# Performance work log

Measured on AMD Instinct MI355X. Metric: run time of the kernel, lower is better.

The kernel has to match this reference:

```python
import jax, jax.numpy as jnp
import numpy as np

N = 50000
E = 1600000
F_IN = 256
DIMS = 64
N_CLS = 16
R = 8


def glorot(key, shape):
    fan = shape[-2] + shape[-1] if len(shape) >= 2 else shape[-1] * 2
    std = jnp.sqrt(6.0 / fan)
    return jax.random.uniform(key, shape, jnp.float32, -std, std)


def setup_inputs() -> dict:
    key = jax.random.key(0)
    ks = jax.random.split(key, 12)
    x = jax.random.normal(ks[0], (N, F_IN), jnp.float32)
    edge_index = jax.random.randint(ks[1], (2, E), 0, N)
    edge_weight = jax.random.uniform(ks[2], (E,), jnp.float32)
    edge_color = jax.random.randint(ks[3], (E,), 0, R)
    W1 = glorot(ks[4], (R, F_IN, DIMS))
    atten1 = glorot(ks[5], (R, 2 * DIMS))
    root1 = glorot(ks[6], (F_IN, DIMS))
    bias1 = jnp.zeros((DIMS,), jnp.float32)
    W2 = glorot(ks[7], (R, DIMS, N_CLS))
    atten2 = glorot(ks[8], (R, 2 * N_CLS))
    root2 = glorot(ks[9], (DIMS, N_CLS))
    bias2 = jnp.zeros((N_CLS,), jnp.float32)
    return dict(x=x, edge_index=edge_index, edge_weight=edge_weight,
                edge_color=edge_color, W1=W1, atten1=atten1, root1=root1,
                bias1=bias1, W2=W2, atten2=atten2, root2=root2, bias2=bias2)


def wrgat_conv(x, src, dst, ew, ec, W, atten, root, bias):
    # x: [N, f_in]; W: [R, f_in, d]; atten: [R, 2d]
    d = W.shape[-1]
    xr = jnp.einsum('nf,rfd->rnd', x, W)            # [R, N, d] per-relation projection
    xi = xr[ec, dst]                                 # [E, d] dst (x_i)
    xj = xr[ec, src]                                 # [E, d] src (x_j)
    a_i = atten[:, :d][ec]                           # [E, d]
    a_j = atten[:, d:][ec]
    s = jnp.sum(a_i * xi + a_j * xj, axis=-1)        # [E]
    s = jax.nn.leaky_relu(s, 0.2)
    # segment softmax over (relation, destination) groups
    seg = ec * N + dst                               # [E], each edge belongs to one relation
    nseg = R * N
    m = jax.ops.segment_max(s, seg, num_segments=nseg)
    m = jnp.where(jnp.isfinite(m), m, 0.0)           # empty segments -> 0
    e = jnp.exp(s - m[seg])
    denom = jax.ops.segment_sum(e, seg, num_segments=nseg)
    alpha = e / jnp.maximum(denom[seg], 1e-16)
    msg = (alpha * ew)[:, None] * xj                 # [E, d]
    summed = jax.ops.segment_sum(msg, seg, num_segments=nseg).reshape(R, N, d)
    cnt = jax.ops.segment_sum(jnp.ones_like(ew), seg, num_segments=nseg).reshape(R, N, 1)
    out = (summed / jnp.maximum(cnt, 1.0)).sum(axis=0)  # mean aggr per relation, summed over relations
    return out + x @ root + bias


def reference(x, edge_index, edge_weight, edge_color, W1, atten1, root1, bias1,
              W2, atten2, root2, bias2):
    src, dst = edge_index[0], edge_index[1]          # PyG flow source_to_target: x_j=src, x_i=dst
    h = wrgat_conv(x, src, dst, edge_weight, edge_color, W1, atten1, root1, bias1)
    h = jax.nn.relu(h)                               # dropout p=0 -> identity
    h = wrgat_conv(h, src, dst, edge_weight, edge_color, W2, atten2, root2, bias2)
    return jax.nn.log_softmax(h, axis=1)
```

## Files before the change

### kernel.cpp

```cpp
#include <hip/hip_runtime.h>
#include <math.h>

#define N_NODES 50000
#define N_EDGES 1600000
#define F_IN    256
#define DIMS    64
#define N_CLS   16
#define R_REL   8
#define CAP     96

#define PROJ_BLKS 3519
#define CSR_BLKS  3125
#define FRONT_BLKS (PROJ_BLKS + CSR_BLKS)

typedef short bf16x8 __attribute__((ext_vector_type(8)));
typedef float f32x4  __attribute__((ext_vector_type(4)));
typedef unsigned int u32;
typedef const __attribute__((address_space(1))) u32* gas_ptr;
typedef __attribute__((address_space(3))) u32* las_ptr;

__device__ __forceinline__ void async16(const void* g, void* l) {
    __builtin_amdgcn_global_load_lds((gas_ptr)g, (las_ptr)l, 16, 0, 0);
}

__device__ __forceinline__ unsigned short f2bf(float f) {
    unsigned u = __float_as_uint(f);
    unsigned r = (u + 0x7fffu + ((u >> 16) & 1u)) >> 16;
    return (unsigned short)r;
}
__device__ __forceinline__ float bf2f(unsigned short u) {
    return __uint_as_float(((unsigned)u) << 16);
}

__global__ __launch_bounds__(256) void cvt_x_kernel(
        const float* __restrict__ x, ushort* __restrict__ xb) {
    int i4 = blockIdx.x * 256 + threadIdx.x;
    float4 v = ((const float4*)x)[i4];
    ushort4 o;
    o.x = f2bf(v.x); o.y = f2bf(v.y); o.z = f2bf(v.z); o.w = f2bf(v.w);
    ((ushort4*)xb)[i4] = o;
}

__global__ __launch_bounds__(256) void cvt_w_kernel(
        const float* __restrict__ W1, const float* __restrict__ root1,
        ushort* __restrict__ wt1) {
    int idx = blockIdx.x * 256 + threadIdx.x;
    int r = idx >> 14, rem = idx & 16383;
    int n = rem >> 8, k = rem & 255;
    float v = (r < 8) ? W1[((size_t)r * F_IN + k) * DIMS + n]
                      : root1[(size_t)k * DIMS + n];
    wt1[idx] = f2bf(v);
}

#define BM 128
__global__ __launch_bounds__(256, 6) void front_kernel(
        const ushort* __restrict__ xb, const ushort* __restrict__ wt1,
        const float* __restrict__ at1,
        ushort* __restrict__ xr1b, float* __restrict__ hroot,
        float* __restrict__ si1, float* __restrict__ sj1,
        const int* __restrict__ ei, const int* __restrict__ ecol,
        const float* __restrict__ ew, int* __restrict__ fill,
        unsigned long long* __restrict__ rec) {
    __shared__ ushort xs[BM * 64];
    const int bid = blockIdx.x;
    const int t = threadIdx.x;

    int pb = -1, cb = -1;
    if (bid < 2 * CSR_BLKS) { if (bid & 1) cb = bid >> 1; else pb = bid >> 1; }
    else pb = CSR_BLKS + (bid - 2 * CSR_BLKS);

    if (cb >= 0) {
        int idx = cb * 256 + t;
        int2  s2 = ((const int2*)ei)[idx];
        int2  d2 = ((const int2*)(ei + N_EDGES))[idx];
        int2  c2 = ((const int2*)ecol)[idx];
        float2 w2 = ((const float2*)ew)[idx];
        int p0 = atomicAdd(&fill[d2.x], 1);
        int p1 = atomicAdd(&fill[d2.y], 1);
        unsigned long long r0 =
            ((unsigned long long)__float_as_uint(w2.x) << 32)
            | (unsigned)(s2.x | (c2.x << 16));
        unsigned long long r1 =
            ((unsigned long long)__float_as_uint(w2.y) << 32)
            | (unsigned)(s2.y | (c2.y << 16));
        int i0 = (p0 < CAP) ? d2.x * CAP + p0 : N_NODES * CAP;
        int i1 = (p1 < CAP) ? d2.y * CAP + p1 : N_NODES * CAP;
        __builtin_nontemporal_store(r0, &rec[i0]);
        __builtin_nontemporal_store(r1, &rec[i1]);
        return;
    }

    const int r = pb / 391;
    const int node0 = (pb % 391) * BM;
    const ushort* wrow = wt1 + (size_t)r * 64 * 256;

    const int w = t >> 6, lane = t & 63;
    const int lane15 = lane & 15, quad = lane >> 4;
    const int row0 = w * 32 + lane15;
    const int sw0 = row0 & 7;

    f32x4 acc[2][4];
    #pragma unroll
    for (int a = 0; a < 2; ++a)
        #pragma unroll
        for (int b = 0; b < 4; ++b)
            acc[a][b] = (f32x4){0.f, 0.f, 0.f, 0.f};

    for (int s = 0; s < 4; ++s) {
        __syncthreads();
        #pragma unroll
        for (int c = 0; c < 4; ++c) {
            int slot = c * 256 + t;
            int row = slot >> 3, k8p = slot & 7;
            int k8 = k8p ^ (row & 7);
            int node = node0 + row;
            if (node >= N_NODES) node = N_NODES - 1;
            async16(&xb[(size_t)node * 256 + s * 64 + k8 * 8],
                    &xs[(c * 256 + w * 64) * 8]);
        }
        __syncthreads();
        #pragma unroll
        for (int kk = 0; kk < 2; ++kk) {
            int k8 = kk * 4 + quad;
            int aidx = row0 * 64 + ((k8 ^ sw0) << 3);
            bf16x8 a0 = *(const bf16x8*)&xs[aidx];
            bf16x8 a1 = *(const bf16x8*)&xs[aidx + 16 * 64];
            int kg = s * 64 + kk * 32 + quad * 8;
            #pragma unroll
            for (int nt = 0; nt < 4; ++nt) {
                bf16x8 b = *(const bf16x8*)&wrow[(size_t)(nt * 16 + lane15) * 256 + kg];
                acc[0][nt] = __builtin_amdgcn_mfma_f32_16x16x32_bf16(a0, b, acc[0][nt], 0, 0, 0);
                acc[1][nt] = __builtin_amdgcn_mfma_f32_16x16x32_bf16(a1, b, acc[1][nt], 0, 0, 0);
            }
        }
    }

    const float* at = at1 + r * 128;
    #pragma unroll
    for (int mt = 0; mt < 2; ++mt) {
        float pi[4] = {0.f, 0.f, 0.f, 0.f};
        float pj[4] = {0.f, 0.f, 0.f, 0.f};
        #pragma unroll
        for (int nt = 0; nt < 4; ++nt) {
            int gcol = nt * 16 + lane15;
            float ai = 0.f, aj = 0.f;
            if (r < 8) { ai = at[gcol]; aj = at[64 + gcol]; }
            #pragma unroll
            for (int reg = 0; reg < 4; ++reg) {
                float v = acc[mt][nt][reg];
                int grow = node0 + w * 32 + mt * 16 + quad * 4 + reg;
                if (grow < N_NODES) {
                    if (r < 8)
                        xr1b[((size_t)r * N_NODES + grow) * 64 + gcol] = f2bf(v);
                    else
                        hroot[(size_t)grow * 64 + gcol] = v;
                }
                pi[reg] += ai * v;
                pj[reg] += aj * v;
            }
        }
        if (r < 8) {
            #pragma unroll
            for (int reg = 0; reg < 4; ++reg) {
                float s_ = pi[reg], u_ = pj[reg];
                #pragma unroll
                for (int off = 1; off < 16; off <<= 1) {
                    s_ += __shfl_xor(s_, off, 64);
                    u_ += __shfl_xor(u_, off, 64);
                }
                if (lane15 == 0) {
                    int grow = node0 + w * 32 + mt * 16 + quad * 4 + reg;
                    if (grow < N_NODES) {
                        si1[r * N_NODES + grow] = s_;
                        sj1[r * N_NODES + grow] = u_;
                    }
                }
            }
        }
    }
}

__global__ __launch_bounds__(256) void agg1s_kernel(
        const unsigned long long* __restrict__ rec, const int* __restrict__ fill,
        const float* __restrict__ si, const float* __restrict__ sj,
        const ushort* __restrict__ xr1b, const float* __restrict__ hroot,
        const float* __restrict__ bias1, float* __restrict__ h) {
    __shared__ int   esrc[4][CAP];
    __shared__ float ecoef[4][CAP];
    __shared__ float sden[4][8];
    __shared__ int   scnt[4][8];
    __shared__ float ssi[4][8];
    const int t = threadIdx.x;
    const int w = t >> 6, lane = t & 63;
    const int d = blockIdx.x * 4 + w;
    if (lane < 8) {
        sden[w][lane] = 0.f; scnt[w][lane] = 0;
        ssi[w][lane] = si[lane * N_NODES + d];
    }
    const int n = min(fill[d], CAP);
    const int base = d * CAP;
    float ex[2] = {0.f, 0.f}, ww[2] = {0.f, 0.f};
    int cc[2] = {0, 0};
    #pragma unroll
    for (int ii = 0; ii < 2; ++ii) {
        int i = lane + ii * 64;
        if (i < n) {
            unsigned long long rv = rec[base + i];
            int px = (int)(unsigned)rv;
            int s = px & 0xffff, c = (px >> 16) & 0x7fff;
            esrc[w][i] = px;
            float sc = ssi[w][c] + sj[c * N_NODES + s];
            sc = sc > 0.f ? sc : 0.2f * sc;
            float e = __expf(sc);
            ex[ii] = e; cc[ii] = c; ww[ii] = __uint_as_float((unsigned)(rv >> 32));
            atomicAdd(&sden[w][c], e);
            atomicAdd(&scnt[w][c], 1);
        }
    }
    #pragma unroll
    for (int ii = 0; ii < 2; ++ii) {
        int i = lane + ii * 64;
        if (i < n)
            ecoef[w][i] = ex[ii] / fmaxf(sden[w][cc[ii]], 1e-16f)
                          * ww[ii] / (float)scnt[w][cc[ii]];
    }
    float a0 = 0.f, a1 = 0.f, a2 = 0.f, a3 = 0.f;
    float a4 = 0.f, a5 = 0.f, a6 = 0.f, a7 = 0.f;
    int i = 0;
    for (; i + 8 <= n; i += 8) {
        int p0 = esrc[w][i],     p1 = esrc[w][i + 1];
        int p2 = esrc[w][i + 2], p3 = esrc[w][i + 3];
        int p4 = esrc[w][i + 4], p5 = esrc[w][i + 5];
        int p6 = esrc[w][i + 6], p7 = esrc[w][i + 7];
        float c0 = ecoef[w][i],     c1 = ecoef[w][i + 1];
        float c2 = ecoef[w][i + 2], c3 = ecoef[w][i + 3];
        float c4 = ecoef[w][i + 4], c5 = ecoef[w][i + 5];
        float c6 = ecoef[w][i + 6], c7 = ecoef[w][i + 7];
        int r0 = (p0 >> 16) * N_NODES + (p0 & 0xffff);
        int r1 = (p1 >> 16) * N_NODES + (p1 & 0xffff);
        int r2 = (p2 >> 16) * N_NODES + (p2 & 0xffff);
        int r3 = (p3 >> 16) * N_NODES + (p3 & 0xffff);
        int r4 = (p4 >> 16) * N_NODES + (p4 & 0xffff);
        int r5 = (p5 >> 16) * N_NODES + (p5 & 0xffff);
        int r6 = (p6 >> 16) * N_NODES + (p6 & 0xffff);
        int r7 = (p7 >> 16) * N_NODES + (p7 & 0xffff);
        a0 += c0 * bf2f(xr1b[(size_t)r0 * 64 + lane]);
        a1 += c1 * bf2f(xr1b[(size_t)r1 * 64 + lane]);
        a2 += c2 * bf2f(xr1b[(size_t)r2 * 64 + lane]);
        a3 += c3 * bf2f(xr1b[(size_t)r3 * 64 + lane]);
        a4 += c4 * bf2f(xr1b[(size_t)r4 * 64 + lane]);
        a5 += c5 * bf2f(xr1b[(size_t)r5 * 64 + lane]);
        a6 += c6 * bf2f(xr1b[(size_t)r6 * 64 + lane]);
        a7 += c7 * bf2f(xr1b[(size_t)r7 * 64 + lane]);
    }
    for (; i < n; ++i) {
        int p0 = esrc[w][i];
        int r0 = (p0 >> 16) * N_NODES + (p0 & 0xffff);
        a0 += ecoef[w][i] * bf2f(xr1b[(size_t)r0 * 64 + lane]);
    }
    float acc = ((a0 + a1) + (a2 + a3)) + ((a4 + a5) + (a6 + a7))
              + hroot[(size_t)d * 64 + lane] + bias1[lane];
    h[(size_t)d * 64 + lane] = fmaxf(acc, 0.f);
}

__global__ __launch_bounds__(256) void proj2_kernel(
        const float* __restrict__ h, const float* __restrict__ W2,
        const float* __restrict__ atten2, ushort* __restrict__ xr2b,
        float* __restrict__ si2, float* __restrict__ sj2) {
    __shared__ float w2sh[8][64][16];
    __shared__ float a2sh[8][32];
    __shared__ float hsh[32][65];
    const int t = threadIdx.x;
    for (int i = t; i < R_REL * DIMS * N_CLS; i += 256)
        w2sh[i >> 10][(i >> 4) & 63][i & 15] = W2[i];
    if (t < R_REL * 2 * N_CLS) a2sh[t >> 5][t & 31] = atten2[t];
    const int node0 = blockIdx.x * 32;
    for (int i = t; i < 32 * 64; i += 256) {
        int nn = i >> 6, kk = i & 63;
        int node = node0 + nn;
        hsh[nn][kk] = (node < N_NODES) ? h[(size_t)node * 64 + kk] : 0.f;
    }
    __syncthreads();
    const int nl = t & 31, r = t >> 5;
    const int node = node0 + nl;
    float acc[16] = {};
    #pragma unroll 4
    for (int k = 0; k < 64; ++k) {
        float hv = hsh[nl][k];
        #pragma unroll
        for (int c = 0; c < 16; ++c) acc[c] += hv * w2sh[r][k][c];
    }
    if (node < N_NODES) {
        float si = 0.f, sj = 0.f;
        size_t base = ((size_t)r * N_NODES + node) * 16;
        #pragma unroll
        for (int c = 0; c < 16; ++c) {
            si += a2sh[r][c] * acc[c];
            sj += a2sh[r][16 + c] * acc[c];
        }
        #pragma unroll
        for (int c4 = 0; c4 < 4; ++c4) {
            ushort4 o;
            o.x = f2bf(acc[c4 * 4 + 0]); o.y = f2bf(acc[c4 * 4 + 1]);
            o.z = f2bf(acc[c4 * 4 + 2]); o.w = f2bf(acc[c4 * 4 + 3]);
            *(ushort4*)&xr2b[base + c4 * 4] = o;
        }
        si2[r * N_NODES + node] = si;
        sj2[r * N_NODES + node] = sj;
    }
}

__global__ __launch_bounds__(256) void agg2s_kernel(
        const unsigned long long* __restrict__ rec, const int* __restrict__ fill,
        const float* __restrict__ si, const float* __restrict__ sj,
        const ushort* __restrict__ xr2b, const float* __restrict__ h,
        const float* __restrict__ root2, const float* __restrict__ bias2,
        float* __restrict__ out) {
    __shared__ float rsh[64][17];
    __shared__ float hsh[4][64];
    __shared__ int   esrc[4][CAP];
    __shared__ float ecoef[4][CAP];
    __shared__ float sden[4][8];
    __shared__ int   scnt[4][8];
    __shared__ float ssi[4][8];
    const int t = threadIdx.x;
    for (int i = t; i < DIMS * N_CLS; i += 256) rsh[i >> 4][i & 15] = root2[i];
    const int w = t >> 6, lane = t & 63;
    const int d = blockIdx.x * 4 + w;
    hsh[w][lane] = h[(size_t)d * 64 + lane];
    if (lane < 8) {
        sden[w][lane] = 0.f; scnt[w][lane] = 0;
        ssi[w][lane] = si[lane * N_NODES + d];
    }
    const int n = min(fill[d], CAP);
    const int base = d * CAP;
    float ex[2] = {0.f, 0.f}, ww[2] = {0.f, 0.f};
    int cc[2] = {0, 0};
    #pragma unroll
    for (int ii = 0; ii < 2; ++ii) {
        int i = lane + ii * 64;
        if (i < n) {
            unsigned long long rv = rec[base + i];
            int px = (int)(unsigned)rv;
            int s = px & 0xffff, c = (px >> 16) & 0x7fff;
            esrc[w][i] = px;
            float sc = ssi[w][c] + sj[c * N_NODES + s];
            sc = sc > 0.f ? sc : 0.2f * sc;
            float e = __expf(sc);
            ex[ii] = e; cc[ii] = c; ww[ii] = __uint_as_float((unsigned)(rv >> 32));
            atomicAdd(&sden[w][c], e);
            atomicAdd(&scnt[w][c], 1);
        }
    }
    #pragma unroll
    for (int ii = 0; ii < 2; ++ii) {
        int i = lane + ii * 64;
        if (i < n)
            ecoef[w][i] = ex[ii] / fmaxf(sden[w][cc[ii]], 1e-16f)
                          * ww[ii] / (float)scnt[w][cc[ii]];
    }
    __syncthreads();
    const int sub = lane >> 4, cd = lane & 15;
    float acc = 0.f, acc2 = 0.f;
    int i = sub;
    for (; i + 4 < n; i += 8) {
        int p0 = esrc[w][i], p1 = esrc[w][i + 4];
        int r0 = (p0 >> 16) * N_NODES + (p0 & 0xffff);
        int r1 = (p1 >> 16) * N_NODES + (p1 & 0xffff);
        acc  += ecoef[w][i]     * bf2f(xr2b[(size_t)r0 * 16 + cd]);
        acc2 += ecoef[w][i + 4] * bf2f(xr2b[(size_t)r1 * 16 + cd]);
    }
    if (i < n) {
        int p = esrc[w][i];
        int row = (p >> 16) * N_NODES + (p & 0xffff);
        acc += ecoef[w][i] * bf2f(xr2b[(size_t)row * 16 + cd]);
    }
    acc += acc2;
    #pragma unroll
    for (int k0 = 0; k0 < 16; ++k0) {
        int k = sub * 16 + k0;
        acc += hsh[w][k] * rsh[k][cd];
    }
    acc += __shfl_xor(acc, 16, 64);
    acc += __shfl_xor(acc, 32, 64);
    if (sub == 0) {
        acc += bias2[cd];
        float m = acc;
        #pragma unroll
        for (int off = 8; off; off >>= 1) m = fmaxf(m, __shfl_xor(m, off, 16));
        float ex2 = expf(acc - m);
        float ssum = ex2;
        #pragma unroll
        for (int off = 8; off; off >>= 1) ssum += __shfl_xor(ssum, off, 16);
        out[(size_t)d * 16 + cd] = acc - m - logf(ssum);
    }
}

extern "C" void kernel_launch(void* const* d_in, const int* in_sizes, int n_in,
                              void* d_out, int out_size, void* d_ws, size_t ws_size,
                              hipStream_t stream) {
    const float* x     = (const float*)d_in[0];
    const int*   ei    = (const int*)  d_in[1];
    const float* ew    = (const float*)d_in[2];
    const int*   ecol  = (const int*)  d_in[3];
    const float* W1    = (const float*)d_in[4];
    const float* at1   = (const float*)d_in[5];
    const float* root1 = (const float*)d_in[6];
    const float* b1    = (const float*)d_in[7];
    const float* W2    = (const float*)d_in[8];
    const float* at2   = (const float*)d_in[9];
    const float* root2 = (const float*)d_in[10];
    const float* b2    = (const float*)d_in[11];
    float* out = (float*)d_out;
    float* ws  = (float*)d_ws;

    ushort*   xb    = (ushort*)(ws + 0);
    ushort*   wt1   = (ushort*)(ws + 6400000);
    ushort*   xr1b  = (ushort*)(ws + 6480000);
    float*    hroot = ws + 19280000;
    ushort*   xr2b  = (ushort*)(ws + 22480000);
    float*    si1   = ws + 25680000;
    float*    sj1   = ws + 26080000;
    float*    si2   = ws + 26480000;
    float*    sj2   = ws + 26880000;
    int*      fill  = (int*)(ws + 27280000);
    float*    h     = ws + 27330000;
    unsigned long long* rec = (unsigned long long*)(ws + 30530000);

    hipMemsetAsync(fill, 0, (size_t)N_NODES * 4, stream);

    cvt_x_kernel<<<12500, 256, 0, stream>>>(x, xb);
    cvt_w_kernel<<<576, 256, 0, stream>>>(W1, root1, wt1);
    front_kernel<<<FRONT_BLKS, 256, 0, stream>>>(xb, wt1, at1, xr1b, hroot,
                                                 si1, sj1, ei, ecol, ew, fill, rec);
    agg1s_kernel<<<12500, 256, 0, stream>>>(rec, fill, si1, sj1, xr1b, hroot, b1, h);
    proj2_kernel<<<1563, 256, 0, stream>>>(h, W2, at2, xr2b, si2, sj2);
    agg2s_kernel<<<12500, 256, 0, stream>>>(rec, fill, si2, sj2, xr2b, h, root2, b2, out);
}
```

Measured before the change: 394.8 us.

## Retile front projection to share each x tile across two relations

Each projection block now handles 64 nodes and up to two relation weight matrices, instead of 128 nodes and one relation. Each x tile loaded into LDS is reused for two relations' MFMAs, and the five relation groups (the last holding only the root projection) replace nine separate passes. This cuts global and LDS traffic for x by roughly half. In exchange the block count changes, per-block work shrinks, and the last group is unbalanced with only one relation.

```diff
diff --git a/kernel.cpp b/kernel.cpp
--- a/kernel.cpp
+++ b/kernel.cpp
@@ -9,7 +9,10 @@
 #define R_REL   8
 #define CAP     96
 
-#define PROJ_BLKS 3519
+#define BM      64
+#define N_TILES 782
+#define N_GRP   5
+#define PROJ_BLKS (N_TILES * N_GRP)
 #define CSR_BLKS  3125
 #define FRONT_BLKS (PROJ_BLKS + CSR_BLKS)
 
@@ -52,7 +55,6 @@
     wt1[idx] = f2bf(v);
 }
 
-#define BM 128
 __global__ __launch_bounds__(256, 6) void front_kernel(
         const ushort* __restrict__ xb, const ushort* __restrict__ wt1,
         const float* __restrict__ at1,
@@ -90,13 +92,14 @@
         return;
     }
 
-    const int r = pb / 391;
-    const int node0 = (pb % 391) * BM;
-    const ushort* wrow = wt1 + (size_t)r * 64 * 256;
+    const int g = pb / N_TILES;
+    const int node0 = (pb % N_TILES) * BM;
+    const int r0g = g * 2;
+    const int nrel = (g < 4) ? 2 : 1;
 
     const int w = t >> 6, lane = t & 63;
     const int lane15 = lane & 15, quad = lane >> 4;
-    const int row0 = w * 32 + lane15;
+    const int row0 = w * 16 + lane15;
     const int sw0 = row0 & 7;
 
     f32x4 acc[2][4];
@@ -109,7 +112,7 @@
     for (int s = 0; s < 4; ++s) {
         __syncthreads();
         #pragma unroll
-        for (int c = 0; c < 4; ++c) {
+        for (int c = 0; c < 2; ++c) {
             int slot = c * 256 + t;
             int row = slot >> 3, k8p = slot & 7;
             int k8 = k8p ^ (row & 7);
@@ -124,20 +127,26 @@
             int k8 = kk * 4 + quad;
             int aidx = row0 * 64 + ((k8 ^ sw0) << 3);
             bf16x8 a0 = *(const bf16x8*)&xs[aidx];
-            bf16x8 a1 = *(const bf16x8*)&xs[aidx + 16 * 64];
             int kg = s * 64 + kk * 32 + quad * 8;
             #pragma unroll
-            for (int nt = 0; nt < 4; ++nt) {
-                bf16x8 b = *(const bf16x8*)&wrow[(size_t)(nt * 16 + lane15) * 256 + kg];
-                acc[0][nt] = __builtin_amdgcn_mfma_f32_16x16x32_bf16(a0, b, acc[0][nt], 0, 0, 0);
-                acc[1][nt] = __builtin_amdgcn_mfma_f32_16x16x32_bf16(a1, b, acc[1][nt], 0, 0, 0);
+            for (int ri = 0; ri < 2; ++ri) {
+                if (ri < nrel) {
+                    const ushort* wrow = wt1 + (size_t)(r0g + ri) * 64 * 256;
+                    #pragma unroll
+                    for (int nt = 0; nt < 4; ++nt) {
+                        bf16x8 b = *(const bf16x8*)&wrow[(size_t)(nt * 16 + lane15) * 256 + kg];
+                        acc[ri][nt] = __builtin_amdgcn_mfma_f32_16x16x32_bf16(a0, b, acc[ri][nt], 0, 0, 0);
+                    }
+                }
             }
         }
     }
 
-    const float* at = at1 + r * 128;
-    #pragma unroll
-    for (int mt = 0; mt < 2; ++mt) {
+    #pragma unroll
+    for (int ri = 0; ri < 2; ++ri) {
+        if (ri >= nrel) break;
+        const int r = r0g + ri;
+        const float* at = at1 + r * 128;
         float pi[4] = {0.f, 0.f, 0.f, 0.f};
         float pj[4] = {0.f, 0.f, 0.f, 0.f};
         #pragma unroll
@@ -147,8 +156,8 @@
             if (r < 8) { ai = at[gcol]; aj = at[64 + gcol]; }
             #pragma unroll
             for (int reg = 0; reg < 4; ++reg) {
-                float v = acc[mt][nt][reg];
-                int grow = node0 + w * 32 + mt * 16 + quad * 4 + reg;
+                float v = acc[ri][nt][reg];
+                int grow = node0 + w * 16 + quad * 4 + reg;
                 if (grow < N_NODES) {
                     if (r < 8)
                         xr1b[((size_t)r * N_NODES + grow) * 64 + gcol] = f2bf(v);
@@ -169,7 +178,7 @@
                     u_ += __shfl_xor(u_, off, 64);
                 }
                 if (lane15 == 0) {
-                    int grow = node0 + w * 32 + mt * 16 + quad * 4 + reg;
+                    int grow = node0 + w * 16 + quad * 4 + reg;
                     if (grow < N_NODES) {
                         si1[r * N_NODES + grow] = s_;
                         sj1[r * N_NODES + grow] = u_;
```

Measured after the change: 470.8 us. 1.19x slower.
